# Kernel tuning notes

Hardware: AMD Instinct MI355X
Metric: run time of the kernel (lower is better)

The kernel has to match this reference:

```python
import jax, jax.numpy as jnp
import numpy as np

N, F_IN, E = 50000, 128, 800000
D1, D2, D3, NUM_LAYERS = 90, 80, 50, 4
EPS = 1e-5


def _gcn_norm(edge_index, n):
    # add self-loops, compute symmetric normalization deg^{-1/2} A_hat deg^{-1/2}
    loops = jnp.arange(n, dtype=edge_index.dtype)
    src = jnp.concatenate([edge_index[0], loops])
    dst = jnp.concatenate([edge_index[1], loops])
    deg = jax.ops.segment_sum(jnp.ones_like(src, dtype=jnp.float32), dst, num_segments=n)
    deg_isqrt = jnp.where(deg > 0, jax.lax.rsqrt(deg), 0.0)
    norm = deg_isqrt[src] * deg_isqrt[dst]  # [E+N]
    return src, dst, norm


def _gcn_conv(x, w, b, src, dst, norm, n):
    h = x @ w                                   # [N, d_out] dense transform first
    msg = h[src] * norm[:, None]                # gather + scale  [E+N, d_out]
    out = jax.ops.segment_sum(msg, dst, num_segments=n)  # scatter-add
    return out + b


def _bn(x, gamma, beta):
    # batch-statistics BatchNorm1d over node dim
    mu = jnp.mean(x, axis=0)
    var = jnp.var(x, axis=0)
    return (x - mu) * jax.lax.rsqrt(var + EPS) * gamma + beta


def setup_inputs() -> dict:
    key = jax.random.key(0)
    ks = jax.random.split(key, 16)
    s = lambda *sh: 1.0 / np.sqrt(sh[0])
    inp = {
        'x': jax.random.normal(ks[0], (N, F_IN), jnp.float32),
        'edge_index': jax.random.randint(ks[1], (2, E), 0, N, dtype=jnp.int32),
        'conv1_w': jax.random.normal(ks[2], (F_IN, D1), jnp.float32) * s(F_IN),
        'conv1_b': jnp.zeros((D1,), jnp.float32),
        'convs_w': jax.random.normal(ks[3], (NUM_LAYERS - 1, D1, D1), jnp.float32) * s(D1),
        'convs_b': jnp.zeros((NUM_LAYERS - 1, D1), jnp.float32),
        'bn1_g': jnp.ones((D1,), jnp.float32), 'bn1_b': jnp.zeros((D1,), jnp.float32),
        'fc1_w': jax.random.normal(ks[4], (D1, D2), jnp.float32) * s(D1),
        'fc1_b': jnp.zeros((D2,), jnp.float32),
        'bn2_g': jnp.ones((D2,), jnp.float32), 'bn2_b': jnp.zeros((D2,), jnp.float32),
        'fc2_w': jax.random.normal(ks[5], (D2, D3), jnp.float32) * s(D2),
        'fc2_b': jnp.zeros((D3,), jnp.float32),
        'bn3_g': jnp.ones((D3,), jnp.float32), 'bn3_b': jnp.zeros((D3,), jnp.float32),
        'fc3_w': jax.random.normal(ks[6], (D3, 1), jnp.float32) * s(D3),
        'fc3_b': jnp.zeros((1,), jnp.float32),
    }
    return inp


def reference(x, edge_index, conv1_w, conv1_b, convs_w, convs_b,
              bn1_g, bn1_b, fc1_w, fc1_b, bn2_g, bn2_b,
              fc2_w, fc2_b, bn3_g, bn3_b, fc3_w, fc3_b):
    n = x.shape[0]
    src, dst, norm = _gcn_norm(edge_index, n)
    h = jax.nn.relu(_gcn_conv(x, conv1_w, conv1_b, src, dst, norm, n))
    for i in range(convs_w.shape[0]):
        h = jax.nn.relu(_gcn_conv(h, convs_w[i], convs_b[i], src, dst, norm, n))
        h = _bn(h, bn1_g, bn1_b)
        # dropout is identity in eval mode
    h = jax.nn.relu(_bn(h @ fc1_w + fc1_b, bn2_g, bn2_b))
    h = jax.nn.relu(_bn(h @ fc2_w + fc2_b, bn3_g, bn3_b))
    return h @ fc3_w + fc3_b
```

## Files before the change

kernel.cpp:

```cpp
#include <hip/hip_runtime.h>

#define NBLK(n, b) (((n) + (b) - 1) / (b))

#define FS 96
#define FS4 24

typedef _Float16 half8_t __attribute__((ext_vector_type(8)));
typedef float float8_t __attribute__((ext_vector_type(8)));
typedef float f32x4_t __attribute__((ext_vector_type(4)));


__global__ void count_k(const int* __restrict__ dst, int* __restrict__ cnt, int e) {
  int i = blockIdx.x * blockDim.x + threadIdx.x;
  if (i < e) atomicAdd(&cnt[dst[i]], 1);
}

__global__ void isq_k(const int* __restrict__ cnt, float* __restrict__ isq, int n) {
  int i = blockIdx.x * blockDim.x + threadIdx.x;
  if (i < n) isq[i] = rsqrtf((float)cnt[i] + 1.0f);
}

__global__ __launch_bounds__(256) void scan1_k(const int* __restrict__ cnt,
                                               int* __restrict__ rowptr,
                                               int* __restrict__ partials, int n) {
  __shared__ int ls[256];
  const int t = threadIdx.x;
  const int base = blockIdx.x * 1024 + t * 4;
  int v0 = 0, v1 = 0, v2 = 0, v3 = 0;
  if (base + 3 < n) {
    int4 q = *reinterpret_cast<const int4*>(cnt + base);
    v0 = q.x; v1 = q.y; v2 = q.z; v3 = q.w;
  } else {
    if (base < n) v0 = cnt[base];
    if (base + 1 < n) v1 = cnt[base + 1];
    if (base + 2 < n) v2 = cnt[base + 2];
  }
  int s = v0 + v1 + v2 + v3;
  ls[t] = s;
  __syncthreads();
  for (int off = 1; off < 256; off <<= 1) {
    int u = (t >= off) ? ls[t - off] : 0;
    __syncthreads();
    ls[t] += u;
    __syncthreads();
  }
  int p = ls[t] - s;
  if (t == 255) partials[blockIdx.x] = ls[255];
  if (base < n) rowptr[base] = p;
  p += v0;
  if (base + 1 < n) rowptr[base + 1] = p;
  p += v1;
  if (base + 2 < n) rowptr[base + 2] = p;
  p += v2;
  if (base + 3 < n) rowptr[base + 3] = p;
}

__global__ __launch_bounds__(256) void scan2_k(const int* __restrict__ partials,
                                               int* __restrict__ offsets, int B) {
  __shared__ int ls[256];
  const int t = threadIdx.x;
  int v = (t < B) ? partials[t] : 0;
  ls[t] = v;
  __syncthreads();
  for (int off = 1; off < 256; off <<= 1) {
    int u = (t >= off) ? ls[t - off] : 0;
    __syncthreads();
    ls[t] += u;
    __syncthreads();
  }
  if (t < B) offsets[t] = ls[t] - v;
  if (t == B - 1) offsets[B] = ls[t];
}

__global__ __launch_bounds__(256) void scan3_k(int* __restrict__ rowptr,
                                               int* __restrict__ cursor,
                                               const int* __restrict__ offsets,
                                               int n, int B) {
  const int t = threadIdx.x;
  const int base = blockIdx.x * 1024 + t * 4;
  const int off = offsets[blockIdx.x];
  if (base + 3 < n) {
    int4 q = *reinterpret_cast<const int4*>(rowptr + base);
    q.x += off; q.y += off; q.z += off; q.w += off;
    *reinterpret_cast<int4*>(rowptr + base) = q;
    *reinterpret_cast<int4*>(cursor + base) = q;
  } else {
    for (int i = base; i < n; ++i) {
      int v = rowptr[i] + off;
      rowptr[i] = v;
      cursor[i] = v;
    }
  }
  if (base == 0 && blockIdx.x == 0) rowptr[n] = offsets[B];
}

__global__ __launch_bounds__(256) void fill_part_k(
    const int* __restrict__ src, const int* __restrict__ dst,
    int* __restrict__ cursor, unsigned short* __restrict__ csr, int e, int n) {
  const int p = blockIdx.x & 7;
  const int q = blockIdx.x >> 3;
  const int nb = gridDim.x >> 3;
  const int ps = (n + 7) >> 3;
  const int lo = p * ps;
  const int hi = min(lo + ps, n);
  const int stride = nb * 256;
  for (int i = q * 256 + threadIdx.x; i < e; i += stride) {
    const int d = dst[i];
    if (d >= lo && d < hi) {
      const int pos = atomicAdd(&cursor[d], 1);
      csr[pos] = (unsigned short)src[i];
    }
  }
}


template <int K, int KP, int M, int INS, int OUTS, int XF, int EPI>
__global__ __launch_bounds__(256, 2) void gemm4_k(
    const float* __restrict__ X, const float* __restrict__ W,
    const float* __restrict__ bias, const float* __restrict__ isq,
    const float* __restrict__ scale, const float* __restrict__ shift,
    void* __restrict__ OUT, int n) {
  constexpr int KG = KP / 8;
  __shared__ _Float16 Wh[6 * KG * 16 * 8];
  const int t = threadIdx.x;
  for (int idx = t; idx < KP * 96; idx += 256) {
    const int k = idx / 96, c = idx - k * 96;
    const float v = (k < K && c < M) ? W[k * M + c] : 0.0f;
    const int tt = c >> 4, cc = c & 15;
    Wh[((tt * KG + (k >> 3)) * 16 + cc) * 8 + (k & 7)] = (_Float16)v;
  }
  __syncthreads();
  const int wid = t >> 6;
  const int lane = t & 63;
  const int lr = lane & 15;
  const int hk = lane >> 4;
  const int r0 = blockIdx.x * 64 + wid * 16;
  const int arow = min(r0 + lr, n - 1);
  const float* __restrict__ xp = X + (size_t)arow * INS;
  const half8_t* __restrict__ Whv = reinterpret_cast<const half8_t*>(Wh);
  f32x4_t acc[6];
#pragma unroll
  for (int tt = 0; tt < 6; ++tt) acc[tt] = (f32x4_t){0.0f, 0.0f, 0.0f, 0.0f};
  for (int ks = 0; ks < KP; ks += 32) {
    const int kb = ks + hk * 8;
    float a[8];
    {
      float4 v0 = *reinterpret_cast<const float4*>(xp + kb);
      float4 v1 = *reinterpret_cast<const float4*>(xp + kb + 4);
      a[0] = v0.x; a[1] = v0.y; a[2] = v0.z; a[3] = v0.w;
      a[4] = v1.x; a[5] = v1.y; a[6] = v1.z; a[7] = v1.w;
    }
    if constexpr (XF == 1) {
#pragma unroll
      for (int i = 0; i < 8; ++i) a[i] = fmaxf(a[i], 0.0f);
    } else if constexpr (XF == 2 || XF == 3) {
      float4 s0 = *reinterpret_cast<const float4*>(scale + kb);
      float4 s1 = *reinterpret_cast<const float4*>(scale + kb + 4);
      float4 h0 = *reinterpret_cast<const float4*>(shift + kb);
      float4 h1 = *reinterpret_cast<const float4*>(shift + kb + 4);
      const float sc[8] = {s0.x, s0.y, s0.z, s0.w, s1.x, s1.y, s1.z, s1.w};
      const float sh[8] = {h0.x, h0.y, h0.z, h0.w, h1.x, h1.y, h1.z, h1.w};
#pragma unroll
      for (int i = 0; i < 8; ++i) {
        if constexpr (XF == 2) a[i] = fmaxf(a[i], 0.0f) * sc[i] + sh[i];
        else a[i] = fmaxf(a[i] * sc[i] + sh[i], 0.0f);
      }
    }
    half8_t af;
#pragma unroll
    for (int i = 0; i < 8; ++i) af[i] = (_Float16)a[i];
    const int kg = kb >> 3;
#pragma unroll
    for (int tt = 0; tt < 6; ++tt) {
      half8_t bf = Whv[(tt * KG + kg) * 16 + lr];
      acc[tt] = __builtin_amdgcn_mfma_f32_16x16x32_f16(af, bf, acc[tt], 0, 0, 0);
    }
  }
  const int rg = r0 + (hk << 2);
  if constexpr (EPI == 0) {
    float siq[4];
#pragma unroll
    for (int j = 0; j < 4; ++j) siq[j] = (rg + j < n) ? isq[rg + j] : 0.0f;
    _Float16* Hh = (_Float16*)OUT;
#pragma unroll
    for (int tt = 0; tt < 6; ++tt) {
      const int c = tt * 16 + lr;
      const int tb = c / 48;
      const int so = c % 48;
#pragma unroll
      for (int j = 0; j < 4; ++j) {
        const int row = rg + j;
        if (row < n)
          Hh[(size_t)tb * n * 48 + (size_t)row * 48 + so] =
              (_Float16)(acc[tt][j] * siq[j]);
      }
    }
  } else {
    float* O = (float*)OUT;
#pragma unroll
    for (int tt = 0; tt < 6; ++tt) {
      const int c = tt * 16 + lr;
      const float bv = (c < M) ? bias[c] : 0.0f;
#pragma unroll
      for (int j = 0; j < 4; ++j) {
        const int row = rg + j;
        if (row < n) O[(size_t)row * OUTS + c] = acc[tt][j] + bv;
      }
    }
  }
}


template <int K, int KP, int M, int MH, int INS, int OUTS, int XF, int EPI>
__global__ __launch_bounds__(256, 2) void gemm2_k(
    const float* __restrict__ X, const float* __restrict__ W,
    const float* __restrict__ bias, const float* __restrict__ isq,
    const float* __restrict__ scale, const float* __restrict__ shift,
    void* __restrict__ OUT, int n) {
  __shared__ float Ws[KP * MH];
  __shared__ float Sc[(XF >= 2) ? KP : 1];
  __shared__ float Sh[(XF >= 2) ? KP : 1];
  const int ms = blockIdx.y;
  for (int idx = threadIdx.x; idx < KP * MH; idx += 256) {
    int k = idx / MH;
    int m = idx - k * MH;
    int col = ms * MH + m;
    Ws[idx] = (k < K && col < M) ? W[k * M + col] : 0.0f;
  }
  if constexpr (XF >= 2) {
    for (int k = threadIdx.x; k < KP; k += 256) {
      Sc[k] = (k < K) ? scale[k] : 0.0f;
      Sh[k] = (k < K) ? shift[k] : 0.0f;
    }
  }
  __syncthreads();
  const int row = blockIdx.x * 256 + threadIdx.x;
  const bool valid = row < n;
  const float* xp = X + (size_t)(valid ? row : 0) * INS;
  float acc[MH];
#pragma unroll
  for (int m = 0; m < MH; ++m) acc[m] = 0.0f;
  for (int k0 = 0; k0 < KP; k0 += 4) {
    float4 tt = *reinterpret_cast<const float4*>(xp + k0);
    float xv[4] = {tt.x, tt.y, tt.z, tt.w};
#pragma unroll
    for (int j = 0; j < 4; ++j) {
      float xval = xv[j];
      if constexpr (XF == 1) xval = fmaxf(xval, 0.0f);
      if constexpr (XF == 2) xval = fmaxf(xval, 0.0f) * Sc[k0 + j] + Sh[k0 + j];
      if constexpr (XF == 3) xval = fmaxf(xval * Sc[k0 + j] + Sh[k0 + j], 0.0f);
      const float* wrow = &Ws[(k0 + j) * MH];
#pragma unroll
      for (int m = 0; m < MH; ++m) acc[m] += xval * wrow[m];
    }
  }
  if (!valid) return;
  float* O = (float*)OUT;
  const size_t base = (size_t)row * OUTS + ms * MH;
#pragma unroll
  for (int m = 0; m < MH; ++m) O[base + m] = acc[m] + bias[ms * MH + m];
}


__global__ __launch_bounds__(256, 6) void gather_k(
    const _Float16* __restrict__ H, const int* __restrict__ rowptr,
    const unsigned short* __restrict__ csr, const float* __restrict__ isq,
    const float* __restrict__ bias, float* __restrict__ A, int n) {
  const int wid = threadIdx.x >> 6;
  const int lane = threadIdx.x & 63;
  const int d = blockIdx.x * 4 + wid;
  if (d >= n) return;
  const int g = lane >> 4;
  const int s = lane & 15;
  const int beg = rowptr[d];
  const int end = rowptr[d + 1];
  const half8_t* __restrict__ Hp = reinterpret_cast<const half8_t*>(H);
  const int sl = (s < 6) ? s : (s - 6);
  const half8_t* __restrict__ lanebase = Hp + ((s < 6) ? 0 : (size_t)n * 6) + sl;
  float8_t acc = {0, 0, 0, 0, 0, 0, 0, 0};
  float8_t acc2 = {0, 0, 0, 0, 0, 0, 0, 0};
  if (lane < 12)
    acc += __builtin_convertvector(lanebase[(size_t)d * 6], float8_t);
  int r = beg + g;
  for (; r + 4 < end; r += 8) {
    const int v0 = (int)csr[r];
    const int v1 = (int)csr[r + 4];
    if (s < 12) {
      acc += __builtin_convertvector(lanebase[(size_t)v0 * 6], float8_t);
      acc2 += __builtin_convertvector(lanebase[(size_t)v1 * 6], float8_t);
    }
  }
  for (; r < end; r += 4) {
    const int v = (int)csr[r];
    if (s < 12) acc += __builtin_convertvector(lanebase[(size_t)v * 6], float8_t);
  }
  acc += acc2;
#pragma unroll
  for (int i = 0; i < 8; ++i) acc[i] += __shfl_xor(acc[i], 16);
#pragma unroll
  for (int i = 0; i < 8; ++i) acc[i] += __shfl_xor(acc[i], 32);
  if (lane < 12) {
    const float sc = isq[d];
    const int c = lane * 8;
    float o[8];
#pragma unroll
    for (int i = 0; i < 8; ++i)
      o[i] = acc[i] * sc + ((c + i < 90) ? bias[c + i] : 0.0f);
    float4* Ap = reinterpret_cast<float4*>(A + (size_t)d * FS + c);
    Ap[0] = make_float4(o[0], o[1], o[2], o[3]);
    Ap[1] = make_float4(o[4], o[5], o[6], o[7]);
  }
}


template <int M, bool RELU>
__global__ __launch_bounds__(256) void bn_stats4_k(const float* __restrict__ X,
                                                   float* __restrict__ gsum,
                                                   float* __restrict__ gsq, int n) {
  __shared__ float ssum[FS];
  __shared__ float ssq[FS];
  for (int i = threadIdx.x; i < FS; i += 256) { ssum[i] = 0.0f; ssq[i] = 0.0f; }
  __syncthreads();
  const int t = threadIdx.x;
  const int cq = t % FS4;
  const int rl = t / FS4;
  constexpr int ROWS = 256 / FS4;
  const float4* __restrict__ Xp = reinterpret_cast<const float4*>(X);
  if (rl < ROWS) {
    float s0 = 0, s1 = 0, s2 = 0, s3 = 0, q0 = 0, q1 = 0, q2 = 0, q3 = 0;
    for (int r = blockIdx.x * ROWS + rl; r < n; r += gridDim.x * ROWS) {
      float4 v = Xp[(size_t)r * FS4 + cq];
      if (RELU) {
        v.x = fmaxf(v.x, 0.0f); v.y = fmaxf(v.y, 0.0f);
        v.z = fmaxf(v.z, 0.0f); v.w = fmaxf(v.w, 0.0f);
      }
      s0 += v.x; q0 += v.x * v.x;
      s1 += v.y; q1 += v.y * v.y;
      s2 += v.z; q2 += v.z * v.z;
      s3 += v.w; q3 += v.w * v.w;
    }
    const int c = cq * 4;
    if (c + 0 < M) { atomicAdd(&ssum[c + 0], s0); atomicAdd(&ssq[c + 0], q0); }
    if (c + 1 < M) { atomicAdd(&ssum[c + 1], s1); atomicAdd(&ssq[c + 1], q1); }
    if (c + 2 < M) { atomicAdd(&ssum[c + 2], s2); atomicAdd(&ssq[c + 2], q2); }
    if (c + 3 < M) { atomicAdd(&ssum[c + 3], s3); atomicAdd(&ssq[c + 3], q3); }
  }
  __syncthreads();
  for (int i = threadIdx.x; i < M; i += 256) {
    atomicAdd(&gsum[i], ssum[i]);
    atomicAdd(&gsq[i], ssq[i]);
  }
}


template <int M>
__global__ void bn_final_k(const float* __restrict__ gsum, const float* __restrict__ gsq,
                           const float* __restrict__ g, const float* __restrict__ b,
                           float* __restrict__ scale, float* __restrict__ shift, float invn) {
  int c = threadIdx.x;
  if (c >= FS) return;
  if (c >= M) { scale[c] = 0.0f; shift[c] = 0.0f; return; }
  float mu = gsum[c] * invn;
  float var = gsq[c] * invn - mu * mu;
  float r = rsqrtf(var + 1e-5f);
  float sc = g[c] * r;
  scale[c] = sc;
  shift[c] = b[c] - mu * sc;
}


extern "C" void kernel_launch(void* const* d_in, const int* in_sizes, int n_in,
                              void* d_out, int out_size, void* d_ws, size_t ws_size,
                              hipStream_t stream) {
  const float* x = (const float*)d_in[0];
  const int* ei = (const int*)d_in[1];
  const float* conv1_w = (const float*)d_in[2];
  const float* conv1_b = (const float*)d_in[3];
  const float* convs_w = (const float*)d_in[4];
  const float* convs_b = (const float*)d_in[5];
  const float* bn1_g = (const float*)d_in[6];
  const float* bn1_b = (const float*)d_in[7];
  const float* fc1_w = (const float*)d_in[8];
  const float* fc1_b = (const float*)d_in[9];
  const float* bn2_g = (const float*)d_in[10];
  const float* bn2_b = (const float*)d_in[11];
  const float* fc2_w = (const float*)d_in[12];
  const float* fc2_b = (const float*)d_in[13];
  const float* bn3_g = (const float*)d_in[14];
  const float* bn3_b = (const float*)d_in[15];
  const float* fc3_w = (const float*)d_in[16];
  const float* fc3_b = (const float*)d_in[17];

  const int N = in_sizes[0] / 128;
  const int E = in_sizes[1] / 2;
  const int* src = ei;
  const int* dst = ei + E;
  const int B = NBLK(N, 1024);

  float* ws = (float*)d_ws;
  float* isq = ws;
  int* rowptr = (int*)(ws + 50048);
  int* cursor = rowptr + 50048;
  int* cnt = cursor + 50048;
  unsigned short* csr16 = (unsigned short*)(cnt + 50048);
  int* partials = (int*)(csr16 + 800000);
  int* offsets = partials + 64;
  float* stats = (float*)(offsets + 128);
  float* scale = stats + 5 * 192;
  float* shift = scale + 96;
  float* bufH = shift + 96;
  float* bufA = bufH + (size_t)N * FS;
  _Float16* bufHh = (_Float16*)bufH;

  float* gs0 = stats + 0 * 192; float* gq0 = gs0 + 96;
  float* gs1 = stats + 1 * 192; float* gq1 = gs1 + 96;
  float* gs2 = stats + 2 * 192; float* gq2 = gs2 + 96;
  float* gs3 = stats + 3 * 192; float* gq3 = gs3 + 96;
  float* gs4 = stats + 4 * 192; float* gq4 = gs4 + 96;

  hipMemsetAsync(cnt, 0, 50048 * sizeof(int), stream);
  hipMemsetAsync(stats, 0, 5 * 192 * sizeof(float), stream);
  count_k<<<NBLK(E, 256), 256, 0, stream>>>(dst, cnt, E);
  isq_k<<<NBLK(N, 256), 256, 0, stream>>>(cnt, isq, N);
  scan1_k<<<B, 256, 0, stream>>>(cnt, rowptr, partials, N);
  scan2_k<<<1, 256, 0, stream>>>(partials, offsets, B);
  scan3_k<<<B, 256, 0, stream>>>(rowptr, cursor, offsets, N, B);
  fill_part_k<<<1024, 256, 0, stream>>>(src, dst, cursor, csr16, E, N);

  const int grows = NBLK(N, 256);
  const int gmf = NBLK(N, 64);
  const int ggath = NBLK(N, 4);
  const float invn = 1.0f / (float)N;

  gemm4_k<128, 128, 90, 128, FS, 0, 0><<<gmf, 256, 0, stream>>>(
      x, conv1_w, nullptr, isq, nullptr, nullptr, bufHh, N);
  gather_k<<<ggath, 256, 0, stream>>>(bufHh, rowptr, csr16, isq, conv1_b, bufA, N);

  gemm4_k<90, 96, 90, FS, FS, 1, 0><<<gmf, 256, 0, stream>>>(
      bufA, convs_w, nullptr, isq, nullptr, nullptr, bufHh, N);
  gather_k<<<ggath, 256, 0, stream>>>(bufHh, rowptr, csr16, isq, convs_b, bufA, N);
  bn_stats4_k<90, true><<<512, 256, 0, stream>>>(bufA, gs0, gq0, N);
  bn_final_k<90><<<1, 128, 0, stream>>>(gs0, gq0, bn1_g, bn1_b, scale, shift, invn);

  gemm4_k<90, 96, 90, FS, FS, 2, 0><<<gmf, 256, 0, stream>>>(
      bufA, convs_w + 90 * 90, nullptr, isq, scale, shift, bufHh, N);
  gather_k<<<ggath, 256, 0, stream>>>(bufHh, rowptr, csr16, isq, convs_b + 90, bufA, N);
  bn_stats4_k<90, true><<<512, 256, 0, stream>>>(bufA, gs1, gq1, N);
  bn_final_k<90><<<1, 128, 0, stream>>>(gs1, gq1, bn1_g, bn1_b, scale, shift, invn);

  gemm4_k<90, 96, 90, FS, FS, 2, 0><<<gmf, 256, 0, stream>>>(
      bufA, convs_w + 2 * 90 * 90, nullptr, isq, scale, shift, bufHh, N);
  gather_k<<<ggath, 256, 0, stream>>>(bufHh, rowptr, csr16, isq, convs_b + 2 * 90, bufA, N);
  bn_stats4_k<90, true><<<512, 256, 0, stream>>>(bufA, gs2, gq2, N);
  bn_final_k<90><<<1, 128, 0, stream>>>(gs2, gq2, bn1_g, bn1_b, scale, shift, invn);

  gemm4_k<90, 96, 80, FS, FS, 2, 1><<<gmf, 256, 0, stream>>>(
      bufA, fc1_w, fc1_b, nullptr, scale, shift, bufH, N);
  bn_stats4_k<80, false><<<512, 256, 0, stream>>>(bufH, gs3, gq3, N);
  bn_final_k<80><<<1, 128, 0, stream>>>(gs3, gq3, bn2_g, bn2_b, scale, shift, invn);

  gemm2_k<80, 80, 50, 25, FS, FS, 3, 1><<<dim3(grows, 2), 256, 0, stream>>>(
      bufH, fc2_w, fc2_b, nullptr, scale, shift, bufA, N);
  bn_stats4_k<50, false><<<512, 256, 0, stream>>>(bufA, gs4, gq4, N);
  bn_final_k<50><<<1, 128, 0, stream>>>(gs4, gq4, bn3_g, bn3_b, scale, shift, invn);

  gemm2_k<50, 52, 1, 1, FS, 1, 3, 1><<<dim3(grows, 1), 256, 0, stream>>>(
      bufA, fc3_w, fc3_b, nullptr, scale, shift, (float*)d_out, N);
}
```

Measured before the change: 498.6 us.

## Fuse BatchNorm statistics into gather and fc1 GEMM epilogues with sliced partials

Computes per-column sum and sum-of-squares for the BN layers inside the gather kernel (over the ReLU'd output) and inside the fc1 GEMM epilogue. Each block accumulates into shared memory, then atomically adds into one of 64 global partial slices, and a new finalize kernel reduces the slices. This removes four separate bn_stats passes that re-read the activation buffer. Gather blocks now process 16 nodes, four per wave, which adds per-element shared-memory atomics and a serial loop per wave.

Result: slower. 582.5 us (+16.8%).

```diff
diff --git a/kernel.cpp b/kernel.cpp
--- a/kernel.cpp
+++ b/kernel.cpp
@@ -114,20 +114,25 @@
 }
 
 
-template <int K, int KP, int M, int INS, int OUTS, int XF, int EPI>
+template <int K, int KP, int M, int INS, int OUTS, int XF, int EPI, bool STATS>
 __global__ __launch_bounds__(256, 2) void gemm4_k(
     const float* __restrict__ X, const float* __restrict__ W,
     const float* __restrict__ bias, const float* __restrict__ isq,
     const float* __restrict__ scale, const float* __restrict__ shift,
-    void* __restrict__ OUT, int n) {
+    void* __restrict__ OUT, float* __restrict__ pstat, int n) {
   constexpr int KG = KP / 8;
   __shared__ _Float16 Wh[6 * KG * 16 * 8];
+  __shared__ float ssum[STATS ? 96 : 1];
+  __shared__ float ssq[STATS ? 96 : 1];
   const int t = threadIdx.x;
   for (int idx = t; idx < KP * 96; idx += 256) {
     const int k = idx / 96, c = idx - k * 96;
     const float v = (k < K && c < M) ? W[k * M + c] : 0.0f;
     const int tt = c >> 4, cc = c & 15;
     Wh[((tt * KG + (k >> 3)) * 16 + cc) * 8 + (k & 7)] = (_Float16)v;
+  }
+  if constexpr (STATS) {
+    if (t < 96) { ssum[t] = 0.0f; ssq[t] = 0.0f; }
   }
   __syncthreads();
   const int wid = t >> 6;
@@ -204,7 +209,24 @@
 #pragma unroll
       for (int j = 0; j < 4; ++j) {
         const int row = rg + j;
-        if (row < n) O[(size_t)row * OUTS + c] = acc[tt][j] + bv;
+        if (row < n) {
+          const float v = acc[tt][j] + bv;
+          O[(size_t)row * OUTS + c] = v;
+          if constexpr (STATS) {
+            if (c < M) {
+              atomicAdd(&ssum[c], v);
+              atomicAdd(&ssq[c], v * v);
+            }
+          }
+        }
+      }
+    }
+    if constexpr (STATS) {
+      __syncthreads();
+      float* P = pstat + (size_t)(blockIdx.x & 63) * 192;
+      for (int i = t; i < 192; i += 256) {
+        const int c = (i < 96) ? i : (i - 96);
+        if (c < M) atomicAdd(&P[i], (i < 96) ? ssum[c] : ssq[c]);
       }
     }
   }
@@ -262,53 +284,80 @@
 }
 
 
+template <bool STATS>
 __global__ __launch_bounds__(256, 6) void gather_k(
     const _Float16* __restrict__ H, const int* __restrict__ rowptr,
     const unsigned short* __restrict__ csr, const float* __restrict__ isq,
-    const float* __restrict__ bias, float* __restrict__ A, int n) {
+    const float* __restrict__ bias, float* __restrict__ A,
+    float* __restrict__ pstat, int n) {
+  __shared__ float ssum[STATS ? FS : 1];
+  __shared__ float ssq[STATS ? FS : 1];
+  if constexpr (STATS) {
+    for (int i = threadIdx.x; i < FS; i += 256) { ssum[i] = 0.0f; ssq[i] = 0.0f; }
+    __syncthreads();
+  }
   const int wid = threadIdx.x >> 6;
   const int lane = threadIdx.x & 63;
-  const int d = blockIdx.x * 4 + wid;
-  if (d >= n) return;
   const int g = lane >> 4;
   const int s = lane & 15;
-  const int beg = rowptr[d];
-  const int end = rowptr[d + 1];
-  const half8_t* __restrict__ Hp = reinterpret_cast<const half8_t*>(H);
   const int sl = (s < 6) ? s : (s - 6);
-  const half8_t* __restrict__ lanebase = Hp + ((s < 6) ? 0 : (size_t)n * 6) + sl;
-  float8_t acc = {0, 0, 0, 0, 0, 0, 0, 0};
-  float8_t acc2 = {0, 0, 0, 0, 0, 0, 0, 0};
-  if (lane < 12)
-    acc += __builtin_convertvector(lanebase[(size_t)d * 6], float8_t);
-  int r = beg + g;
-  for (; r + 4 < end; r += 8) {
-    const int v0 = (int)csr[r];
-    const int v1 = (int)csr[r + 4];
-    if (s < 12) {
-      acc += __builtin_convertvector(lanebase[(size_t)v0 * 6], float8_t);
-      acc2 += __builtin_convertvector(lanebase[(size_t)v1 * 6], float8_t);
-    }
-  }
-  for (; r < end; r += 4) {
-    const int v = (int)csr[r];
-    if (s < 12) acc += __builtin_convertvector(lanebase[(size_t)v * 6], float8_t);
-  }
-  acc += acc2;
-#pragma unroll
-  for (int i = 0; i < 8; ++i) acc[i] += __shfl_xor(acc[i], 16);
-#pragma unroll
-  for (int i = 0; i < 8; ++i) acc[i] += __shfl_xor(acc[i], 32);
-  if (lane < 12) {
-    const float sc = isq[d];
-    const int c = lane * 8;
-    float o[8];
-#pragma unroll
-    for (int i = 0; i < 8; ++i)
-      o[i] = acc[i] * sc + ((c + i < 90) ? bias[c + i] : 0.0f);
-    float4* Ap = reinterpret_cast<float4*>(A + (size_t)d * FS + c);
-    Ap[0] = make_float4(o[0], o[1], o[2], o[3]);
-    Ap[1] = make_float4(o[4], o[5], o[6], o[7]);
+  for (int it = 0; it < 4; ++it) {
+    const int d = blockIdx.x * 16 + wid * 4 + it;
+    if (d >= n) continue;
+    const int beg = rowptr[d];
+    const int end = rowptr[d + 1];
+    const half8_t* __restrict__ Hp = reinterpret_cast<const half8_t*>(H);
+    const half8_t* __restrict__ lanebase =
+        Hp + ((s < 6) ? 0 : (size_t)n * 6) + sl;
+    float8_t acc = {0, 0, 0, 0, 0, 0, 0, 0};
+    float8_t acc2 = {0, 0, 0, 0, 0, 0, 0, 0};
+    if (lane < 12)
+      acc += __builtin_convertvector(lanebase[(size_t)d * 6], float8_t);
+    int r = beg + g;
+    for (; r + 4 < end; r += 8) {
+      const int v0 = (int)csr[r];
+      const int v1 = (int)csr[r + 4];
+      if (s < 12) {
+        acc += __builtin_convertvector(lanebase[(size_t)v0 * 6], float8_t);
+        acc2 += __builtin_convertvector(lanebase[(size_t)v1 * 6], float8_t);
+      }
+    }
+    for (; r < end; r += 4) {
+      const int v = (int)csr[r];
+      if (s < 12) acc += __builtin_convertvector(lanebase[(size_t)v * 6], float8_t);
+    }
+    acc += acc2;
+#pragma unroll
+    for (int i = 0; i < 8; ++i) acc[i] += __shfl_xor(acc[i], 16);
+#pragma unroll
+    for (int i = 0; i < 8; ++i) acc[i] += __shfl_xor(acc[i], 32);
+    if (lane < 12) {
+      const float sc = isq[d];
+      const int c = lane * 8;
+      float o[8];
+#pragma unroll
+      for (int i = 0; i < 8; ++i)
+        o[i] = acc[i] * sc + ((c + i < 90) ? bias[c + i] : 0.0f);
+      float4* Ap = reinterpret_cast<float4*>(A + (size_t)d * FS + c);
+      Ap[0] = make_float4(o[0], o[1], o[2], o[3]);
+      Ap[1] = make_float4(o[4], o[5], o[6], o[7]);
+      if constexpr (STATS) {
+#pragma unroll
+        for (int i = 0; i < 8; ++i) {
+          const float v = fmaxf(o[i], 0.0f);
+          atomicAdd(&ssum[c + i], v);
+          atomicAdd(&ssq[c + i], v * v);
+        }
+      }
+    }
+  }
+  if constexpr (STATS) {
+    __syncthreads();
+    float* P = pstat + (size_t)(blockIdx.x & 63) * 192;
+    for (int i = threadIdx.x; i < 192; i += 256) {
+      const int c = (i < 96) ? i : (i - 96);
+      if (c < 90) atomicAdd(&P[i], (i < 96) ? ssum[c] : ssq[c]);
+    }
   }
 }
 
@@ -362,6 +411,27 @@
   if (c >= M) { scale[c] = 0.0f; shift[c] = 0.0f; return; }
   float mu = gsum[c] * invn;
   float var = gsq[c] * invn - mu * mu;
+  float r = rsqrtf(var + 1e-5f);
+  float sc = g[c] * r;
+  scale[c] = sc;
+  shift[c] = b[c] - mu * sc;
+}
+
+template <int M>
+__global__ void bn_final2_k(const float* __restrict__ P,
+                            const float* __restrict__ g, const float* __restrict__ b,
+                            float* __restrict__ scale, float* __restrict__ shift,
+                            float invn) {
+  int c = threadIdx.x;
+  if (c >= FS) return;
+  if (c >= M) { scale[c] = 0.0f; shift[c] = 0.0f; return; }
+  float s = 0.0f, q = 0.0f;
+  for (int sl = 0; sl < 64; ++sl) {
+    s += P[sl * 192 + c];
+    q += P[sl * 192 + 96 + c];
+  }
+  float mu = s * invn;
+  float var = q * invn - mu * mu;
   float r = rsqrtf(var + 1e-5f);
   float sc = g[c] * r;
   scale[c] = sc;
@@ -406,20 +476,23 @@
   int* partials = (int*)(csr16 + 800000);
   int* offsets = partials + 64;
   float* stats = (float*)(offsets + 128);
-  float* scale = stats + 5 * 192;
+  float* scale = stats + 192;
   float* shift = scale + 96;
-  float* bufH = shift + 96;
+  float* pst = shift + 96;
+  float* bufH = pst + 4 * 64 * 192;
   float* bufA = bufH + (size_t)N * FS;
   _Float16* bufHh = (_Float16*)bufH;
 
-  float* gs0 = stats + 0 * 192; float* gq0 = gs0 + 96;
-  float* gs1 = stats + 1 * 192; float* gq1 = gs1 + 96;
-  float* gs2 = stats + 2 * 192; float* gq2 = gs2 + 96;
-  float* gs3 = stats + 3 * 192; float* gq3 = gs3 + 96;
-  float* gs4 = stats + 4 * 192; float* gq4 = gs4 + 96;
+  float* P0 = pst + 0 * 64 * 192;
+  float* P1 = pst + 1 * 64 * 192;
+  float* P2 = pst + 2 * 64 * 192;
+  float* P3 = pst + 3 * 64 * 192;
+  float* gs4 = stats;
+  float* gq4 = stats + 96;
 
   hipMemsetAsync(cnt, 0, 50048 * sizeof(int), stream);
-  hipMemsetAsync(stats, 0, 5 * 192 * sizeof(float), stream);
+  hipMemsetAsync(stats, 0, 192 * sizeof(float), stream);
+  hipMemsetAsync(pst, 0, 4 * 64 * 192 * sizeof(float), stream);
   count_k<<<NBLK(E, 256), 256, 0, stream>>>(dst, cnt, E);
   isq_k<<<NBLK(N, 256), 256, 0, stream>>>(cnt, isq, N);
   scan1_k<<<B, 256, 0, stream>>>(cnt, rowptr, partials, N);
@@ -429,35 +502,35 @@
 
   const int grows = NBLK(N, 256);
   const int gmf = NBLK(N, 64);
-  const int ggath = NBLK(N, 4);
+  const int ggath = NBLK(N, 16);
   const float invn = 1.0f / (float)N;
 
-  gemm4_k<128, 128, 90, 128, FS, 0, 0><<<gmf, 256, 0, stream>>>(
-      x, conv1_w, nullptr, isq, nullptr, nullptr, bufHh, N);
-  gather_k<<<ggath, 256, 0, stream>>>(bufHh, rowptr, csr16, isq, conv1_b, bufA, N);
-
-  gemm4_k<90, 96, 90, FS, FS, 1, 0><<<gmf, 256, 0, stream>>>(
-      bufA, convs_w, nullptr, isq, nullptr, nullptr, bufHh, N);
-  gather_k<<<ggath, 256, 0, stream>>>(bufHh, rowptr, csr16, isq, convs_b, bufA, N);
-  bn_stats4_k<90, true><<<512, 256, 0, stream>>>(bufA, gs0, gq0, N);
-  bn_final_k<90><<<1, 128, 0, stream>>>(gs0, gq0, bn1_g, bn1_b, scale, shift, invn);
-
-  gemm4_k<90, 96, 90, FS, FS, 2, 0><<<gmf, 256, 0, stream>>>(
-      bufA, convs_w + 90 * 90, nullptr, isq, scale, shift, bufHh, N);
-  gather_k<<<ggath, 256, 0, stream>>>(bufHh, rowptr, csr16, isq, convs_b + 90, bufA, N);
-  bn_stats4_k<90, true><<<512, 256, 0, stream>>>(bufA, gs1, gq1, N);
-  bn_final_k<90><<<1, 128, 0, stream>>>(gs1, gq1, bn1_g, bn1_b, scale, shift, invn);
-
-  gemm4_k<90, 96, 90, FS, FS, 2, 0><<<gmf, 256, 0, stream>>>(
-      bufA, convs_w + 2 * 90 * 90, nullptr, isq, scale, shift, bufHh, N);
-  gather_k<<<ggath, 256, 0, stream>>>(bufHh, rowptr, csr16, isq, convs_b + 2 * 90, bufA, N);
-  bn_stats4_k<90, true><<<512, 256, 0, stream>>>(bufA, gs2, gq2, N);
-  bn_final_k<90><<<1, 128, 0, stream>>>(gs2, gq2, bn1_g, bn1_b, scale, shift, invn);
-
-  gemm4_k<90, 96, 80, FS, FS, 2, 1><<<gmf, 256, 0, stream>>>(
-      bufA, fc1_w, fc1_b, nullptr, scale, shift, bufH, N);
-  bn_stats4_k<80, false><<<512, 256, 0, stream>>>(bufH, gs3, gq3, N);
-  bn_final_k<80><<<1, 128, 0, stream>>>(gs3, gq3, bn2_g, bn2_b, scale, shift, invn);
+  gemm4_k<128, 128, 90, 128, FS, 0, 0, false><<<gmf, 256, 0, stream>>>(
+      x, conv1_w, nullptr, isq, nullptr, nullptr, bufHh, nullptr, N);
+  gather_k<false><<<ggath, 256, 0, stream>>>(bufHh, rowptr, csr16, isq, conv1_b,
+                                             bufA, nullptr, N);
+
+  gemm4_k<90, 96, 90, FS, FS, 1, 0, false><<<gmf, 256, 0, stream>>>(
+      bufA, convs_w, nullptr, isq, nullptr, nullptr, bufHh, nullptr, N);
+  gather_k<true><<<ggath, 256, 0, stream>>>(bufHh, rowptr, csr16, isq, convs_b,
+                                            bufA, P0, N);
+  bn_final2_k<90><<<1, 128, 0, stream>>>(P0, bn1_g, bn1_b, scale, shift, invn);
+
+  gemm4_k<90, 96, 90, FS, FS, 2, 0, false><<<gmf, 256, 0, stream>>>(
+      bufA, convs_w + 90 * 90, nullptr, isq, scale, shift, bufHh, nullptr, N);
+  gather_k<true><<<ggath, 256, 0, stream>>>(bufHh, rowptr, csr16, isq, convs_b + 90,
+                                            bufA, P1, N);
+  bn_final2_k<90><<<1, 128, 0, stream>>>(P1, bn1_g, bn1_b, scale, shift, invn);
+
+  gemm4_k<90, 96, 90, FS, FS, 2, 0, false><<<gmf, 256, 0, stream>>>(
+      bufA, convs_w + 2 * 90 * 90, nullptr, isq, scale, shift, bufHh, nullptr, N);
+  gather_k<true><<<ggath, 256, 0, stream>>>(bufHh, rowptr, csr16, isq, convs_b + 2 * 90,
+                                            bufA, P2, N);
+  bn_final2_k<90><<<1, 128, 0, stream>>>(P2, bn1_g, bn1_b, scale, shift, invn);
+
+  gemm4_k<90, 96, 80, FS, FS, 2, 1, true><<<gmf, 256, 0, stream>>>(
+      bufA, fc1_w, fc1_b, nullptr, scale, shift, bufH, P3, N);
+  bn_final2_k<80><<<1, 128, 0, stream>>>(P3, bn2_g, bn2_b, scale, shift, invn);
 
   gemm2_k<80, 80, 50, 25, FS, FS, 3, 1><<<dim3(grows, 2), 256, 0, stream>>>(
       bufH, fc2_w, fc2_b, nullptr, scale, shift, bufA, N);
```
